# Kernel tuning notes

Measured on AMD Instinct MI355X. Metric: run time of the kernel, lower is better.

The kernel has to match this reference:

```python
import jax, jax.numpy as jnp
import numpy as np

NUM_GRAPHS = 64


def setup_inputs() -> dict:
    key = jax.random.key(0)
    ks = jax.random.split(key, 6)
    N, E, D, H = 100000, 1600000, 512, 128
    x = jax.random.normal(ks[0], (N, D), dtype=jnp.float32)
    edge_index = jax.random.randint(ks[1], (2, E), 0, N, dtype=jnp.int64)
    batch = jnp.sort(jax.random.randint(ks[2], (N,), 0, NUM_GRAPHS, dtype=jnp.int64))
    W1 = jax.random.normal(ks[3], (D, H), dtype=jnp.float32) * (1.0 / np.sqrt(D))
    b1 = jnp.zeros((H,), dtype=jnp.float32)
    W2 = jax.random.normal(ks[4], (H, H), dtype=jnp.float32) * (1.0 / np.sqrt(H))
    b2 = jnp.zeros((H,), dtype=jnp.float32)
    return {"x": x, "edge_index": edge_index, "batch": batch,
            "W1": W1, "b1": b1, "W2": W2, "b2": b2}


def _gcn_conv(x, row, col, norm, n_nodes, W, b):
    # PyG GCNConv: transform, then D^{-1/2}(A+I)D^{-1/2} propagate, then bias.
    h = x @ W                                   # [N, H]
    msg = h[row] * norm[:, None]                # gather + edge normalize
    out = jax.ops.segment_sum(msg, col, num_segments=n_nodes)  # scatter-add
    return out + b


def reference(x, edge_index, batch, W1, b1, W2, b2):
    N = x.shape[0]
    loop = jnp.arange(N, dtype=edge_index.dtype)
    row = jnp.concatenate([edge_index[0], loop])  # sources (with self loops)
    col = jnp.concatenate([edge_index[1], loop])  # targets
    deg = jax.ops.segment_sum(jnp.ones_like(col, dtype=x.dtype), col,
                              num_segments=N)
    dinv = jnp.where(deg > 0, jax.lax.rsqrt(deg), 0.0)
    norm = dinv[row] * dinv[col]

    h = jax.nn.relu(_gcn_conv(x, row, col, norm, N, W1, b1))
    h = jax.nn.relu(_gcn_conv(h, row, col, norm, N, W2, b2))

    # global_mean_pool over batch segment ids
    sums = jax.ops.segment_sum(h, batch, num_segments=NUM_GRAPHS)
    cnts = jax.ops.segment_sum(jnp.ones((N,), dtype=h.dtype), batch,
                               num_segments=NUM_GRAPHS)
    pooled = sums / jnp.maximum(cnts, 1.0)[:, None]
    # dropout is identity in eval mode
    return pooled
```

## Files before the change

### kernel.cpp

```cpp
#include <hip/hip_runtime.h>
#include <hip/hip_bf16.h>

typedef __attribute__((ext_vector_type(8))) short short8;
typedef __attribute__((ext_vector_type(4))) float f32x4;

__device__ __forceinline__ ushort f2b(float f) {
    union { float f; uint u; } v; v.f = f;
    uint u = v.u;
    u += 0x7fffu + ((u >> 16) & 1u);
    return (ushort)(u >> 16);
}
__device__ __forceinline__ float blo(uint u) { return __uint_as_float(u << 16); }
__device__ __forceinline__ float bhi(uint u) { return __uint_as_float(u & 0xffff0000u); }

__device__ __forceinline__ void gl_lds16(const void* g, void* s) {
    __builtin_amdgcn_global_load_lds(
        (const __attribute__((address_space(1))) void*)g,
        (__attribute__((address_space(3))) void*)s, 16, 0, 0);
}

#define ECAP 32768
#define CCAP 40960


__global__ __launch_bounds__(256) void k_setup_scatter(
    const float4* __restrict__ x4, uint2* __restrict__ xb2, int total4, int cvb,
    const float* __restrict__ W1, ushort* __restrict__ wt1b, int D,
    const float* __restrict__ W2, ushort* __restrict__ wt2b, int H,
    const int* __restrict__ batch, int N, int G, int* __restrict__ gstart,
    float* __restrict__ psum, float* __restrict__ dinv, uint* __restrict__ hb0zrow,
    const int* __restrict__ ei, int E, int NB, int* __restrict__ bcur,
    uint* __restrict__ ebuf, int c1b, int c2b, int bb) {
    __shared__ int h[128], gb[128], lc[128];
    int b = blockIdx.x, t = threadIdx.x;
    if (b < cvb) {
        int base = b * 4096 + t;
#pragma unroll
        for (int u = 0; u < 16; u += 8) {
            float4 v[8];
#pragma unroll
            for (int j = 0; j < 8; ++j) {
                int idx = base + (u + j) * 256;
                v[j] = (idx < total4) ? x4[idx] : make_float4(0.f, 0.f, 0.f, 0.f);
            }
#pragma unroll
            for (int j = 0; j < 8; ++j) {
                int idx = base + (u + j) * 256;
                if (idx < total4) {
                    uint2 p;
                    p.x = ((uint)f2b(v[j].y) << 16) | (uint)f2b(v[j].x);
                    p.y = ((uint)f2b(v[j].w) << 16) | (uint)f2b(v[j].z);
                    xb2[idx] = p;
                }
            }
        }
    } else if (b < cvb + c1b) {
        int o = (b - cvb) * 256 + t;
        if (o < 128 * D) {
            int n = o / D, k = o - n * D;
            wt1b[o] = f2b(W1[(size_t)k * 128 + n]);
        }
    } else if (b < cvb + c1b + c2b) {
        int o = (b - cvb - c1b) * 256 + t;
        if (o < 128 * H) {
            int n = o / H, k = o - n * H;
            wt2b[o] = f2b(W2[(size_t)k * 128 + n]);
        }
    } else if (b < cvb + c1b + c2b + bb) {
        int i = (b - cvb - c1b - c2b) * 256 + t;
        if (i < N) {
            int bt = batch[i];
            int prev = (i == 0) ? -1 : batch[i - 1];
            for (int g = prev + 1; g <= bt; ++g) gstart[g] = i;
            if (i == N - 1)
                for (int g = bt + 1; g <= G; ++g) gstart[g] = N;
        }
    } else if (b == cvb + c1b + c2b + bb) {
        for (int i = t; i < G * H; i += 256) psum[i] = 0.f;
        if (t == 0) dinv[N] = 0.f;
        for (int i = t; i < 64; i += 256) hb0zrow[i] = 0u;
    } else {
        int sb = b - (cvb + c1b + c2b + bb + 1);
        if (t < 128) { h[t] = 0; lc[t] = 0; }
        __syncthreads();
        int e0 = sb * 2048;
        int r[8], c[8], bk[8];
#pragma unroll
        for (int u = 0; u < 8; ++u) {
            int e = e0 + u * 256 + t;
            if (e < E) {
                r[u] = ei[e];
                c[u] = ei[E + e];
                bk[u] = c[u] >> 10;
                atomicAdd(&h[bk[u]], 1);
            }
        }
        __syncthreads();
        if (t < NB && h[t]) gb[t] = atomicAdd(&bcur[t], h[t]);
        __syncthreads();
#pragma unroll
        for (int u = 0; u < 8; ++u) {
            int e = e0 + u * 256 + t;
            if (e < E) {
                int p = gb[bk[u]] + atomicAdd(&lc[bk[u]], 1);
                ebuf[(size_t)bk[u] * ECAP + p] = ((uint)(c[u] & 1023) << 22) | (uint)r[u];
            }
        }
    }
}


__global__ __launch_bounds__(256) void k_bucket_sort(const uint* __restrict__ ebuf,
                                                     const int* __restrict__ bcur,
                                                     int N, int NB,
                                                     uint* __restrict__ offs,
                                                     float* __restrict__ dinv,
                                                     int* __restrict__ csr) {
    __shared__ int cnt[1024];
    __shared__ int cur[1024];
    __shared__ int wsum[4];
    int t = threadIdx.x;
    int b = blockIdx.x;
    int node0 = b << 10;
    int nn = min(1024, N - node0);
    for (int i = t; i < nn; i += 256) cnt[i] = 0;
    __syncthreads();
    int e0 = b * ECAP, e1 = e0 + bcur[b];
    int e0p = b * CCAP;
    for (int e = e0 + t; e < e1; e += 256) atomicAdd(&cnt[ebuf[e] >> 22], 1);
    __syncthreads();
    int i0 = t * 4;
    int x[4], px[4];
#pragma unroll
    for (int j = 0; j < 4; ++j) {
        x[j] = (i0 + j < nn) ? cnt[i0 + j] : 0;
        px[j] = (x[j] + 7) & ~7;
    }
    int tot = px[0] + px[1] + px[2] + px[3];
    int run = tot;
    int lane = t & 63, w = t >> 6;
#pragma unroll
    for (int off = 1; off < 64; off <<= 1) {
        int v = __shfl_up(run, off);
        if (lane >= off) run += v;
    }
    if (lane == 63) wsum[w] = run;
    __syncthreads();
    int base = 0;
    for (int u = 0; u < w; ++u) base += wsum[u];
    base += run - tot;
#pragma unroll
    for (int j = 0; j < 4; ++j) {
        if (i0 + j < nn) {
            int node = node0 + i0 + j;
            offs[node] = ((uint)(e0p + base) << 10) | (uint)x[j];
            cur[i0 + j] = base;
            dinv[node] = rsqrtf((float)(x[j] + 1));
            for (int k = x[j]; k < px[j]; ++k) csr[e0p + base + k] = N;
            base += px[j];
        }
    }
    __syncthreads();
    for (int e = e0 + t; e < e1; e += 256) {
        uint v = ebuf[e];
        int p = atomicAdd(&cur[v >> 22], 1);
        csr[e0p + p] = (int)(v & 0x3FFFFFu);
    }
}


template <int NT, bool SCALE>
__global__ __launch_bounds__(256) void k_gemm(
    const ushort* __restrict__ A, const ushort* __restrict__ Wt,
    const float* __restrict__ dinv, ushort* __restrict__ outb, int N) {
    constexpr int K = NT * 64;
    __shared__ __align__(16) char asb[128 * 64 * 2];
    __shared__ __align__(16) char bsb[128 * 64 * 2];
    const int tid = threadIdx.x;
    const int row0 = blockIdx.x * 128;
    const int w = tid >> 6, l = tid & 63;
    const int lr = l & 15, lk = l >> 4;
    f32x4 acc[2][8] = {};

    for (int t = 0; t < NT; ++t) {
        const int kb = t * 64;
#pragma unroll
        for (int i = 0; i < 4; ++i) {
            int b = (w << 12) + (i << 10) + (l << 4);
            int r = b >> 7, cb = b & 127;
            int sb = cb ^ ((r & 7) << 4);
            int gr = row0 + r;
            if (gr < N)
                gl_lds16((const char*)A + ((size_t)gr * K + kb) * 2 + sb,
                         asb + (w << 12) + (i << 10));
        }
#pragma unroll
        for (int i = 0; i < 4; ++i) {
            int b = (w << 12) + (i << 10) + (l << 4);
            int r = b >> 7, cb = b & 127;
            int sb = cb ^ ((r & 7) << 4);
            gl_lds16((const char*)Wt + ((size_t)r * K + kb) * 2 + sb,
                     bsb + (w << 12) + (i << 10));
        }
        __syncthreads();
        const int wr0 = w * 32;
#pragma unroll
        for (int ks = 0; ks < 2; ++ks) {
            const int r0 = wr0 + lr, r1 = wr0 + 16 + lr;
            const int c0 = ks * 64 + lk * 16;
            short8 a0 = *(const short8*)(asb + (r0 << 7) + (c0 ^ ((r0 & 7) << 4)));
            short8 a1 = *(const short8*)(asb + (r1 << 7) + (c0 ^ ((r1 & 7) << 4)));
#pragma unroll
            for (int nf = 0; nf < 8; ++nf) {
                const int nr = nf * 16 + lr;
                short8 bf = *(const short8*)(bsb + (nr << 7) + (c0 ^ ((nr & 7) << 4)));
                acc[0][nf] = __builtin_amdgcn_mfma_f32_16x16x32_bf16(a0, bf, acc[0][nf], 0, 0, 0);
                acc[1][nf] = __builtin_amdgcn_mfma_f32_16x16x32_bf16(a1, bf, acc[1][nf], 0, 0, 0);
            }
        }
        __syncthreads();
    }
#pragma unroll
    for (int mf = 0; mf < 2; ++mf) {
#pragma unroll
        for (int r = 0; r < 4; ++r) {
            int row = row0 + w * 32 + mf * 16 + lk * 4 + r;
            if (row < N) {
                float dv = 1.f;
                if constexpr (SCALE) dv = dinv[row];
#pragma unroll
                for (int nf = 0; nf < 8; ++nf)
                    outb[(size_t)row * 128 + nf * 16 + lr] = f2b(acc[mf][nf][r] * dv);
            }
        }
    }
}


#define ACC8(v) { a[0] += blo(v.x); a[1] += bhi(v.x); a[2] += blo(v.y); a[3] += bhi(v.y); \
                  a[4] += blo(v.z); a[5] += bhi(v.z); a[6] += blo(v.w); a[7] += bhi(v.w); }

template <int POOL>
__global__ __launch_bounds__(256) void k_spmm(
    const uint4* __restrict__ hs4, const int* __restrict__ csr,
    const uint* __restrict__ offs, const float* __restrict__ dinv,
    const float* __restrict__ bias, uint4* __restrict__ outb,
    float* __restrict__ psum, const int* __restrict__ batch, int N) {
    __shared__ float4 pacc[POOL ? 16 : 1][32];
    __shared__ int gid[POOL ? 16 : 1];
    const int grp = threadIdx.x >> 4, ql = threadIdx.x & 15;
    const int node = blockIdx.x * 16 + grp;
    const bool active = node < N;
    float a[8] = {};
    int beg = 0, pend = 0;
    if (active) {
        uint pv = offs[node];
        beg = (int)(pv >> 10);
        pend = beg + (((int)(pv & 1023u) + 7) & ~7);
        uint4 s = hs4[(size_t)node * 16 + ql];
        ACC8(s)
    }
    int i = beg;
    for (; i + 16 <= pend; i += 16) {
        int4 s0 = *(const int4*)(csr + i);
        int4 s1 = *(const int4*)(csr + i + 4);
        int4 s2 = *(const int4*)(csr + i + 8);
        int4 s3 = *(const int4*)(csr + i + 12);
        uint4 v0 = hs4[(size_t)s0.x * 16 + ql];
        uint4 v1 = hs4[(size_t)s0.y * 16 + ql];
        uint4 v2 = hs4[(size_t)s0.z * 16 + ql];
        uint4 v3 = hs4[(size_t)s0.w * 16 + ql];
        uint4 v4 = hs4[(size_t)s1.x * 16 + ql];
        uint4 v5 = hs4[(size_t)s1.y * 16 + ql];
        uint4 v6 = hs4[(size_t)s1.z * 16 + ql];
        uint4 v7 = hs4[(size_t)s1.w * 16 + ql];
        uint4 v8 = hs4[(size_t)s2.x * 16 + ql];
        uint4 v9 = hs4[(size_t)s2.y * 16 + ql];
        uint4 va = hs4[(size_t)s2.z * 16 + ql];
        uint4 vb = hs4[(size_t)s2.w * 16 + ql];
        uint4 vc = hs4[(size_t)s3.x * 16 + ql];
        uint4 vd = hs4[(size_t)s3.y * 16 + ql];
        uint4 ve = hs4[(size_t)s3.z * 16 + ql];
        uint4 vf = hs4[(size_t)s3.w * 16 + ql];
        ACC8(v0) ACC8(v1) ACC8(v2) ACC8(v3) ACC8(v4) ACC8(v5) ACC8(v6) ACC8(v7)
        ACC8(v8) ACC8(v9) ACC8(va) ACC8(vb) ACC8(vc) ACC8(vd) ACC8(ve) ACC8(vf)
    }
    if (i < pend) {
        int4 s0 = *(const int4*)(csr + i);
        int4 s1 = *(const int4*)(csr + i + 4);
        uint4 v0 = hs4[(size_t)s0.x * 16 + ql];
        uint4 v1 = hs4[(size_t)s0.y * 16 + ql];
        uint4 v2 = hs4[(size_t)s0.z * 16 + ql];
        uint4 v3 = hs4[(size_t)s0.w * 16 + ql];
        uint4 v4 = hs4[(size_t)s1.x * 16 + ql];
        uint4 v5 = hs4[(size_t)s1.y * 16 + ql];
        uint4 v6 = hs4[(size_t)s1.z * 16 + ql];
        uint4 v7 = hs4[(size_t)s1.w * 16 + ql];
        ACC8(v0) ACC8(v1) ACC8(v2) ACC8(v3) ACC8(v4) ACC8(v5) ACC8(v6) ACC8(v7)
    }
    float o[8] = {};
    if (active) {
        float dv = dinv[node];
        float4 b0 = ((const float4*)bias)[ql * 2];
        float4 b1 = ((const float4*)bias)[ql * 2 + 1];
        o[0] = fmaxf(fmaf(a[0], dv, b0.x), 0.f);
        o[1] = fmaxf(fmaf(a[1], dv, b0.y), 0.f);
        o[2] = fmaxf(fmaf(a[2], dv, b0.z), 0.f);
        o[3] = fmaxf(fmaf(a[3], dv, b0.w), 0.f);
        o[4] = fmaxf(fmaf(a[4], dv, b1.x), 0.f);
        o[5] = fmaxf(fmaf(a[5], dv, b1.y), 0.f);
        o[6] = fmaxf(fmaf(a[6], dv, b1.z), 0.f);
        o[7] = fmaxf(fmaf(a[7], dv, b1.w), 0.f);
    }
    if constexpr (POOL) {
        pacc[grp][ql * 2]     = make_float4(o[0], o[1], o[2], o[3]);
        pacc[grp][ql * 2 + 1] = make_float4(o[4], o[5], o[6], o[7]);
        if (ql == 0) gid[grp] = active ? batch[node] : -1;
        __syncthreads();
        int t = threadIdx.x;
        if (t < 128) {
            float run = 0.f; int prev = -1;
#pragma unroll
            for (int g2 = 0; g2 < 16; ++g2) {
                int g = gid[g2];
                if (g < 0) continue;
                if (g != prev && prev >= 0) { atomicAdd(&psum[prev * 128 + t], run); run = 0.f; }
                run += ((const float*)pacc[g2])[t];
                prev = g;
            }
            if (prev >= 0) atomicAdd(&psum[prev * 128 + t], run);
        }
    } else {
        if (active) {
            uint4 ov;
            ov.x = ((uint)f2b(o[1]) << 16) | (uint)f2b(o[0]);
            ov.y = ((uint)f2b(o[3]) << 16) | (uint)f2b(o[2]);
            ov.z = ((uint)f2b(o[5]) << 16) | (uint)f2b(o[4]);
            ov.w = ((uint)f2b(o[7]) << 16) | (uint)f2b(o[6]);
            outb[(size_t)node * 16 + ql] = ov;
        }
    }
}


__global__ void k_div(const float* __restrict__ psum, const int* __restrict__ gstart,
                      float* __restrict__ out, int total) {
    int i = blockIdx.x * blockDim.x + threadIdx.x;
    if (i < total) {
        int g = i >> 7;
        float c = (float)(gstart[g + 1] - gstart[g]);
        out[i] = psum[i] / fmaxf(c, 1.f);
    }
}


extern "C" void kernel_launch(void* const* d_in, const int* in_sizes, int n_in,
                              void* d_out, int out_size, void* d_ws, size_t ws_size,
                              hipStream_t stream) {
    const float* x     = (const float*)d_in[0];
    const int*   ei    = (const int*)d_in[1];
    const int*   batch = (const int*)d_in[2];
    const float* W1    = (const float*)d_in[3];
    const float* b1    = (const float*)d_in[4];
    const float* W2    = (const float*)d_in[5];
    const float* b2    = (const float*)d_in[6];
    float* outp = (float*)d_out;

    const int N = in_sizes[2];
    const int E = in_sizes[1] / 2;
    const int D = in_sizes[0] / N;
    const int H = in_sizes[4];
    const int G = out_size / H;
    const int NB = (N + 1023) >> 10;

    char* ws = (char*)d_ws;
    size_t off = 0;
    auto alloc = [&](size_t bytes) -> char* {
        char* p = ws + off;
        off = (off + bytes + 255) & ~(size_t)255;
        return p;
    };
    float*  dinv    = (float*)alloc((size_t)(N + 1) * 4);
    uint*   offs    = (uint*)alloc((size_t)N * 4);
    int*    gstart  = (int*)alloc((size_t)(G + 1) * 4);
    float*  psum    = (float*)alloc((size_t)G * H * 4);
    int*    bcur    = (int*)alloc(128 * 4);
    ushort* wt1b    = (ushort*)alloc((size_t)H * D * 2);
    ushort* wt2b    = (ushort*)alloc((size_t)H * H * 2);
    int*    csr     = (int*)alloc((size_t)NB * CCAP * 4);
    uint*   ebuf    = (uint*)alloc((size_t)NB * ECAP * 4);
    ushort* xb      = (ushort*)alloc((size_t)N * D * 2);
    char*   hbase   = alloc(((size_t)N * 2 + 8) * H * 2);
    ushort* hb0     = (ushort*)hbase;
    ushort* hb1     = (ushort*)(hbase + ((size_t)N + 8) * H * 2);
    (void)ws_size; (void)n_in;

    hipMemsetAsync(bcur, 0, 128 * 4, stream);

    int total4 = (N * D) / 4;
    int cvb = (total4 + 4095) / 4096;
    int c1b = (128 * D + 255) / 256;
    int c2b = (128 * H + 255) / 256;
    int bb  = (N + 255) / 256;
    int scb = (E + 2047) / 2048;

    k_setup_scatter<<<cvb + c1b + c2b + bb + 1 + scb, 256, 0, stream>>>(
        (const float4*)x, (uint2*)xb, total4, cvb,
        W1, wt1b, D, W2, wt2b, H, batch, N, G, gstart, psum, dinv,
        (uint*)(hb0 + (size_t)N * H), ei, E, NB, bcur, ebuf, c1b, c2b, bb);

    k_bucket_sort<<<NB, 256, 0, stream>>>(ebuf, bcur, N, NB, offs, dinv, csr);

    int gblocks = (N + 127) / 128;
    int sblocks = (N + 15) / 16;
    k_gemm<8, true><<<gblocks, 256, 0, stream>>>(xb, wt1b, dinv, hb0, N);
    k_spmm<0><<<sblocks, 256, 0, stream>>>(
        (const uint4*)hb0, csr, offs, dinv, b1, (uint4*)hb1, nullptr, nullptr, N);
    k_gemm<2, true><<<gblocks, 256, 0, stream>>>(hb1, wt2b, dinv, hb0, N);
    k_spmm<1><<<sblocks, 256, 0, stream>>>(
        (const uint4*)hb0, csr, offs, dinv, b2, nullptr, psum, batch, N);
    k_div<<<(G * H + 255) / 256, 256, 0, stream>>>(psum, gstart, outp, G * H);
}
```

Before: 284.5 us.

## Fuse fp32-to-bf16 conversion of x into first GEMM with resident W1 in LDS

Removes the separate pass that converted x from fp32 to a bf16 copy in the setup kernel. The first GEMM now reads fp32 x directly from global memory, converts it to bf16 in registers, and keeps all of transposed W1 resident in 128 KB of LDS. It uses 32x32x16 MFMA with 512-thread blocks and register prefetch of A. This avoids writing and re-reading about 100 MB of bf16 x, at the cost of large LDS use per block (low occupancy) and uncoalesced per-row A loads.

```diff
diff --git a/kernel.cpp b/kernel.cpp
--- a/kernel.cpp
+++ b/kernel.cpp
@@ -3,6 +3,7 @@
 
 typedef __attribute__((ext_vector_type(8))) short short8;
 typedef __attribute__((ext_vector_type(4))) float f32x4;
+typedef __attribute__((ext_vector_type(16))) float f32x16;
 
 __device__ __forceinline__ ushort f2b(float f) {
     union { float f; uint u; } v; v.f = f;
@@ -24,7 +25,6 @@
 
 
 __global__ __launch_bounds__(256) void k_setup_scatter(
-    const float4* __restrict__ x4, uint2* __restrict__ xb2, int total4, int cvb,
     const float* __restrict__ W1, ushort* __restrict__ wt1b, int D,
     const float* __restrict__ W2, ushort* __restrict__ wt2b, int H,
     const int* __restrict__ batch, int N, int G, int* __restrict__ gstart,
@@ -33,41 +33,20 @@
     uint* __restrict__ ebuf, int c1b, int c2b, int bb) {
     __shared__ int h[128], gb[128], lc[128];
     int b = blockIdx.x, t = threadIdx.x;
-    if (b < cvb) {
-        int base = b * 4096 + t;
-#pragma unroll
-        for (int u = 0; u < 16; u += 8) {
-            float4 v[8];
-#pragma unroll
-            for (int j = 0; j < 8; ++j) {
-                int idx = base + (u + j) * 256;
-                v[j] = (idx < total4) ? x4[idx] : make_float4(0.f, 0.f, 0.f, 0.f);
-            }
-#pragma unroll
-            for (int j = 0; j < 8; ++j) {
-                int idx = base + (u + j) * 256;
-                if (idx < total4) {
-                    uint2 p;
-                    p.x = ((uint)f2b(v[j].y) << 16) | (uint)f2b(v[j].x);
-                    p.y = ((uint)f2b(v[j].w) << 16) | (uint)f2b(v[j].z);
-                    xb2[idx] = p;
-                }
-            }
-        }
-    } else if (b < cvb + c1b) {
-        int o = (b - cvb) * 256 + t;
+    if (b < c1b) {
+        int o = b * 256 + t;
         if (o < 128 * D) {
             int n = o / D, k = o - n * D;
             wt1b[o] = f2b(W1[(size_t)k * 128 + n]);
         }
-    } else if (b < cvb + c1b + c2b) {
-        int o = (b - cvb - c1b) * 256 + t;
+    } else if (b < c1b + c2b) {
+        int o = (b - c1b) * 256 + t;
         if (o < 128 * H) {
             int n = o / H, k = o - n * H;
             wt2b[o] = f2b(W2[(size_t)k * 128 + n]);
         }
-    } else if (b < cvb + c1b + c2b + bb) {
-        int i = (b - cvb - c1b - c2b) * 256 + t;
+    } else if (b < c1b + c2b + bb) {
+        int i = (b - c1b - c2b) * 256 + t;
         if (i < N) {
             int bt = batch[i];
             int prev = (i == 0) ? -1 : batch[i - 1];
@@ -75,12 +54,12 @@
             if (i == N - 1)
                 for (int g = bt + 1; g <= G; ++g) gstart[g] = N;
         }
-    } else if (b == cvb + c1b + c2b + bb) {
+    } else if (b == c1b + c2b + bb) {
         for (int i = t; i < G * H; i += 256) psum[i] = 0.f;
         if (t == 0) dinv[N] = 0.f;
         for (int i = t; i < 64; i += 256) hb0zrow[i] = 0u;
     } else {
-        int sb = b - (cvb + c1b + c2b + bb + 1);
+        int sb = b - (c1b + c2b + bb + 1);
         if (t < 128) { h[t] = 0; lc[t] = 0; }
         __syncthreads();
         int e0 = sb * 2048;
@@ -169,8 +148,80 @@
 }
 
 
-template <int NT, bool SCALE>
-__global__ __launch_bounds__(256) void k_gemm(
+__global__ __launch_bounds__(512, 2) void k_gemm1(
+    const float* __restrict__ A, const ushort* __restrict__ Wt,
+    const float* __restrict__ dinv, ushort* __restrict__ outb, int N) {
+    __shared__ __align__(16) char bsb[128 * 1024];
+    const int tid = threadIdx.x;
+    {
+        const uint4* w4 = (const uint4*)Wt;
+#pragma unroll
+        for (int i = 0; i < 16; i += 8) {
+            uint4 v[8];
+#pragma unroll
+            for (int j = 0; j < 8; ++j) v[j] = w4[(i + j) * 512 + tid];
+#pragma unroll
+            for (int j = 0; j < 8; ++j) {
+                int f = (i + j) * 512 + tid;
+                int n = f >> 6, g = f & 63;
+                *(uint4*)(bsb + n * 1024 + ((g ^ (n & 7)) << 4)) = v[j];
+            }
+        }
+    }
+    __syncthreads();
+    const int w = tid >> 6, l = tid & 63;
+    const int rl = l & 31;
+    const int kh = l >> 5;
+    const int row0 = blockIdx.x * 256 + w * 32;
+    int arow = row0 + rl;
+    int arow_c = (arow < N) ? arow : 0;
+    const float* Arow = A + (size_t)arow_c * 512 + kh * 8;
+    const char* bB[4];
+#pragma unroll
+    for (int nf = 0; nf < 4; ++nf) bB[nf] = bsb + (nf * 32 + rl) * 1024;
+    const int bx = (rl & 7) << 4;
+
+    f32x16 acc[4] = {};
+    float4 af[4][2];
+#pragma unroll
+    for (int p = 0; p < 4; ++p) {
+        af[p][0] = *(const float4*)(Arow + p * 16);
+        af[p][1] = *(const float4*)(Arow + p * 16 + 4);
+    }
+#pragma unroll
+    for (int t = 0; t < 32; ++t) {
+        float4 v0 = af[t & 3][0], v1 = af[t & 3][1];
+        if (t + 4 < 32) {
+            af[t & 3][0] = *(const float4*)(Arow + (t + 4) * 16);
+            af[t & 3][1] = *(const float4*)(Arow + (t + 4) * 16 + 4);
+        }
+        short8 a;
+        a[0] = (short)f2b(v0.x); a[1] = (short)f2b(v0.y);
+        a[2] = (short)f2b(v0.z); a[3] = (short)f2b(v0.w);
+        a[4] = (short)f2b(v1.x); a[5] = (short)f2b(v1.y);
+        a[6] = (short)f2b(v1.z); a[7] = (short)f2b(v1.w);
+        const int goff = (2 * t + kh) << 4;
+#pragma unroll
+        for (int nf = 0; nf < 4; ++nf) {
+            short8 bf = *(const short8*)(bB[nf] + (goff ^ bx));
+            acc[nf] = __builtin_amdgcn_mfma_f32_32x32x16_bf16(a, bf, acc[nf], 0, 0, 0);
+        }
+    }
+#pragma unroll
+    for (int r = 0; r < 16; ++r) {
+        int grow = row0 + (r & 3) + 8 * (r >> 2) + 4 * kh;
+        if (grow < N) {
+            float dv = dinv[grow];
+#pragma unroll
+            for (int nf = 0; nf < 4; ++nf)
+                outb[(size_t)grow * 128 + nf * 32 + rl] = f2b(acc[nf][r] * dv);
+        }
+    }
+}
+
+
+template <int NT>
+__global__ __launch_bounds__(256) void k_gemm2(
     const ushort* __restrict__ A, const ushort* __restrict__ Wt,
     const float* __restrict__ dinv, ushort* __restrict__ outb, int N) {
     constexpr int K = NT * 64;
@@ -226,8 +277,7 @@
         for (int r = 0; r < 4; ++r) {
             int row = row0 + w * 32 + mf * 16 + lk * 4 + r;
             if (row < N) {
-                float dv = 1.f;
-                if constexpr (SCALE) dv = dinv[row];
+                float dv = dinv[row];
 #pragma unroll
                 for (int nf = 0; nf < 8; ++nf)
                     outb[(size_t)row * 128 + nf * 16 + lr] = f2b(acc[mf][nf][r] * dv);
@@ -389,7 +439,6 @@
     ushort* wt2b    = (ushort*)alloc((size_t)H * H * 2);
     int*    csr     = (int*)alloc((size_t)NB * CCAP * 4);
     uint*   ebuf    = (uint*)alloc((size_t)NB * ECAP * 4);
-    ushort* xb      = (ushort*)alloc((size_t)N * D * 2);
     char*   hbase   = alloc(((size_t)N * 2 + 8) * H * 2);
     ushort* hb0     = (ushort*)hbase;
     ushort* hb1     = (ushort*)(hbase + ((size_t)N + 8) * H * 2);
@@ -397,26 +446,24 @@
 
     hipMemsetAsync(bcur, 0, 128 * 4, stream);
 
-    int total4 = (N * D) / 4;
-    int cvb = (total4 + 4095) / 4096;
     int c1b = (128 * D + 255) / 256;
     int c2b = (128 * H + 255) / 256;
     int bb  = (N + 255) / 256;
     int scb = (E + 2047) / 2048;
 
-    k_setup_scatter<<<cvb + c1b + c2b + bb + 1 + scb, 256, 0, stream>>>(
-        (const float4*)x, (uint2*)xb, total4, cvb,
+    k_setup_scatter<<<c1b + c2b + bb + 1 + scb, 256, 0, stream>>>(
         W1, wt1b, D, W2, wt2b, H, batch, N, G, gstart, psum, dinv,
         (uint*)(hb0 + (size_t)N * H), ei, E, NB, bcur, ebuf, c1b, c2b, bb);
 
     k_bucket_sort<<<NB, 256, 0, stream>>>(ebuf, bcur, N, NB, offs, dinv, csr);
 
-    int gblocks = (N + 127) / 128;
-    int sblocks = (N + 15) / 16;
-    k_gemm<8, true><<<gblocks, 256, 0, stream>>>(xb, wt1b, dinv, hb0, N);
+    int g1blocks = (N + 255) / 256;
+    int g2blocks = (N + 127) / 128;
+    int sblocks  = (N + 15) / 16;
+    k_gemm1<<<g1blocks, 512, 0, stream>>>(x, wt1b, dinv, hb0, N);
     k_spmm<0><<<sblocks, 256, 0, stream>>>(
         (const uint4*)hb0, csr, offs, dinv, b1, (uint4*)hb1, nullptr, nullptr, N);
-    k_gemm<2, true><<<gblocks, 256, 0, stream>>>(hb1, wt2b, dinv, hb0, N);
+    k_gemm2<2><<<g2blocks, 256, 0, stream>>>(hb1, wt2b, dinv, hb0, N);
     k_spmm<1><<<sblocks, 256, 0, stream>>>(
         (const uint4*)hb0, csr, offs, dinv, b2, nullptr, psum, batch, N);
     k_div<<<(G * H + 255) / 256, 256, 0, stream>>>(psum, gstart, outp, G * H);
```

Result: faster. 266.8 us (-6.2%).
